# Performance work log

Measured on AMD Instinct MI355X. Metric: run time of the kernel, lower is better.

Reference implementation:

```python
import jax, jax.numpy as jnp
import numpy as np

NEG_SLOPE = 0.2  # PyG GATConv default LeakyReLU slope


def _gat(h, src, dst, num_nodes, W, a_src, a_dst, bias):
    """PyG-style GATConv (concat=True, eval mode, self-loops already in src/dst)."""
    heads, out = a_src.shape
    hp = (h @ W).reshape(num_nodes, heads, out)          # (N, H, F)
    e_s = (hp * a_src).sum(-1)                            # (N, H)
    e_d = (hp * a_dst).sum(-1)                            # (N, H)
    e = jax.nn.leaky_relu(e_s[src] + e_d[dst], NEG_SLOPE)  # (E, H)
    m = jax.ops.segment_max(e, dst, num_segments=num_nodes)
    w = jnp.exp(e - m[dst])
    z = jax.ops.segment_sum(w, dst, num_segments=num_nodes)
    alpha = w / (z[dst] + 1e-16)                          # softmax over in-edges per dst
    agg = jax.ops.segment_sum(hp[src] * alpha[:, :, None], dst, num_segments=num_nodes)
    return agg.reshape(num_nodes, heads * out) + bias


def setup_inputs() -> dict:
    key = jax.random.key(0)
    ks = jax.random.split(key, 20)
    N, T, Fin, H, heads, E = 30000, 4, 256, 64, 4, 240000
    D = H * heads  # 256
    s = 0.05
    p = lambda k, shape: (jax.random.normal(k, shape, jnp.float32) * s)
    return {
        "x": jax.random.normal(ks[0], (N, T, Fin), jnp.float32),
        "edge_index": jax.random.randint(ks[1], (2, E), 0, N, jnp.int32),
        "Wp": p(ks[2], (Fin, H)), "bp": p(ks[3], (H,)),
        "W0": p(ks[4], (H, D)), "a_src0": p(ks[5], (heads, H)), "a_dst0": p(ks[6], (heads, H)), "b0": p(ks[7], (D,)),
        "W1": p(ks[8], (D, D)), "a_src1": p(ks[9], (heads, H)), "a_dst1": p(ks[10], (heads, H)), "b1": p(ks[11], (D,)),
        "Wq": p(ks[12], (D, D)), "bq": p(ks[13], (D,)),
        "Wk": p(ks[14], (D, D)), "bk": p(ks[15], (D,)),
        "Wv": p(ks[16], (D, D)), "bv": p(ks[17], (D,)),
    }


def reference(x, edge_index, Wp, bp, W0, a_src0, a_dst0, b0, W1, a_src1, a_dst1, b1,
              Wq, bq, Wk, bk, Wv, bv):
    N, T, Fin = x.shape
    D = Wq.shape[0]
    loops = jnp.arange(N, dtype=edge_index.dtype)
    src = jnp.concatenate([edge_index[0], loops])  # add self-loops (PyG default)
    dst = jnp.concatenate([edge_index[1], loops])
    xT = jnp.transpose(x, (1, 0, 2))  # (T, N, Fin)

    def step(_, xt):
        h = xt @ Wp + bp
        h = jax.nn.elu(_gat(h, src, dst, N, W0, a_src0, a_dst0, b0))
        h = jax.nn.elu(_gat(h, src, dst, N, W1, a_src1, a_dst1, b1))
        return None, h

    _, embs = jax.lax.scan(step, None, xT)  # (T, N, D)

    # temporal attention
    Q = embs @ Wq + bq
    K = embs @ Wk + bk
    V = embs @ Wv + bv
    Q_time = Q.mean(axis=1)  # (T, D)
    K_time = K.mean(axis=1)  # (T, D)
    scores = (Q_time @ K_time.T) / jnp.sqrt(jnp.asarray(D, jnp.float32))
    attn = jax.nn.softmax(scores, axis=1)            # (T, T)
    Vr = V.reshape(T, -1)                            # (T, N*D)
    attended = attn @ Vr                             # (T, N*D)
    return attended[-1].reshape(N, D)
```

## Files before the change

### kernel.cpp

```cpp
#include <hip/hip_runtime.h>
#include <math.h>

#define NEG_SLOPE 0.2f

typedef __attribute__((ext_vector_type(8))) short short8;
typedef __attribute__((ext_vector_type(4))) float f32x4;

__device__ inline unsigned short f2bf(float f){
  union { float f; unsigned u; } v; v.f = f;
  unsigned r = v.u + 0x7fffu + ((v.u >> 16) & 1u);
  return (unsigned short)(r >> 16);
}
__device__ inline float bf2f(unsigned u){
  union { unsigned u; float f; } v; v.u = u << 16; return v.f;
}

__global__ __launch_bounds__(256) void k_deg_count(const int* __restrict__ dst, int E, int* __restrict__ deg){
  int i = blockIdx.x*256 + threadIdx.x;
  if (i < E) atomicAdd(&deg[dst[i]], 1);
}
__global__ __launch_bounds__(256) void k_scan_blk(const int* __restrict__ deg, int* __restrict__ rowptr,
                                                  int* __restrict__ bsum, int N){
  __shared__ int ws[4];
  int tid = threadIdx.x;
  int i = blockIdx.x*256 + tid;
  int v = (i < N) ? deg[i]+1 : 0;
  int lane = tid & 63, w = tid >> 6;
  int s = v;
  #pragma unroll
  for (int off=1; off<64; off<<=1){
    int u = __shfl_up(s, off);
    if (lane >= off) s += u;
  }
  if (lane == 63) ws[w] = s;
  __syncthreads();
  int woff = 0;
  #pragma unroll
  for (int k=0;k<4;k++) if (k < w) woff += ws[k];
  int incl = s + woff;
  if (i < N) rowptr[i] = incl - v;
  if (tid == 255) bsum[blockIdx.x] = incl;
}
__global__ __launch_bounds__(256) void k_scan_top(int* __restrict__ bsum, int nb, int* __restrict__ rowptrN){
  __shared__ int buf[256];
  int tid = threadIdx.x;
  int v = (tid < nb) ? bsum[tid] : 0;
  buf[tid] = v;
  __syncthreads();
  for (int off=1; off<256; off<<=1){
    int add = (tid >= off) ? buf[tid-off] : 0;
    __syncthreads();
    buf[tid] += add;
    __syncthreads();
  }
  if (tid < nb) bsum[tid] = buf[tid] - v;
  if (tid == 0) rowptrN[0] = buf[255];
}
__global__ __launch_bounds__(256) void k_scan_fix(int* __restrict__ rowptr, const int* __restrict__ bsum,
                                                  int* __restrict__ pos, int* __restrict__ colidx, int N){
  int i = blockIdx.x*256 + threadIdx.x;
  if (i < N){
    int r = rowptr[i] + bsum[blockIdx.x];
    rowptr[i] = r;
    colidx[r] = i;
    pos[i] = r + 1;
  }
}
__global__ __launch_bounds__(256) void k_fill_edges(const int* __restrict__ src, const int* __restrict__ dst,
                                                    int E, int* __restrict__ pos, int* __restrict__ colidx){
  int i = blockIdx.x*256 + threadIdx.x;
  if (i < E){
    int d = dst[i];
    colidx[atomicAdd(&pos[d],1)] = src[i];
  }
}

__global__ __launch_bounds__(256) void k_prep(const float* __restrict__ Wp, const float* __restrict__ W0,
                                              const float* __restrict__ W1, const float* __restrict__ Wv,
                                              const float* __restrict__ as0, const float* __restrict__ ad0,
                                              unsigned short* __restrict__ WpT, unsigned short* __restrict__ W0T4,
                                              unsigned short* __restrict__ W1T, unsigned short* __restrict__ WvT,
                                              float* __restrict__ ahs, float* __restrict__ ahd){
  int idx = blockIdx.x*256 + threadIdx.x;
  if (idx < 16384){
    int k = idx >> 6, p = idx & 63;
    WpT[p*256 + k] = f2bf(Wp[idx]);
  } else if (idx < 32768){
    int i = idx - 16384;
    int h = i >> 12, r = i & 4095, p = r >> 6, k = r & 63;
    W0T4[i] = f2bf(W0[k*256 + h*64 + p]);
  } else if (idx < 98304){
    int i = idx - 32768; int k = i >> 8, p = i & 255;
    W1T[p*256 + k] = f2bf(W1[i]);
  } else if (idx < 163840){
    int i = idx - 98304; int k = i >> 8, p = i & 255;
    WvT[p*256 + k] = f2bf(Wv[i]);
  } else if (idx < 164096){
    int i = idx - 163840;
    int h = i >> 6, d = i & 63;
    float ss = 0.f, sd = 0.f;
    for (int j=0;j<64;j++){
      float w = W0[d*256 + h*64 + j];
      ss += w * as0[h*64 + j];
      sd += w * ad0[h*64 + j];
    }
    ahs[i] = ss; ahd[i] = sd;
  }
}

__global__ __launch_bounds__(256) void k_h0(const float* __restrict__ A,
                                            const unsigned short* __restrict__ Bt,
                                            const float* __restrict__ bias,
                                            unsigned short* __restrict__ C, int M, int Nn){
  int wid = blockIdx.x*4 + (threadIdx.x >> 6);
  int m0 = wid * 64;
  if (m0 >= M) return;
  int lane = threadIdx.x & 63;
  int lr = lane & 15, g = lane >> 4, lk = g*8;
  const float* Arow[4];
  #pragma unroll
  for (int m=0;m<4;m++){
    int row = m0 + m*16 + lr;
    if (row > M-1) row = M-1;
    Arow[m] = A + (size_t)row*256 + lk;
  }
  const unsigned short* Bb = Bt + (size_t)lr*256 + lk;
  f32x4 acc[4][4];
  #pragma unroll
  for (int m=0;m<4;m++)
    #pragma unroll
    for (int n=0;n<4;n++)
      #pragma unroll
      for (int j=0;j<4;j++) acc[m][n][j] = 0.f;

  #pragma unroll 2
  for (int ks=0; ks<8; ks++){
    int k0 = ks*32;
    short8 bfr[4];
    #pragma unroll
    for (int n=0;n<4;n++)
      bfr[n] = *(const short8*)(Bb + (size_t)n*16*256 + k0);
    short8 afr[4];
    #pragma unroll
    for (int m=0;m<4;m++){
      float4 u = *(const float4*)(Arow[m] + k0);
      float4 w = *(const float4*)(Arow[m] + k0 + 4);
      afr[m][0]=(short)f2bf(u.x); afr[m][1]=(short)f2bf(u.y);
      afr[m][2]=(short)f2bf(u.z); afr[m][3]=(short)f2bf(u.w);
      afr[m][4]=(short)f2bf(w.x); afr[m][5]=(short)f2bf(w.y);
      afr[m][6]=(short)f2bf(w.z); afr[m][7]=(short)f2bf(w.w);
    }
    #pragma unroll
    for (int m=0;m<4;m++)
      #pragma unroll
      for (int n=0;n<4;n++)
        acc[m][n] = __builtin_amdgcn_mfma_f32_16x16x32_bf16(afr[m], bfr[n], acc[m][n], 0,0,0);
  }
  #pragma unroll
  for (int n=0;n<4;n++){
    int col = n*16 + lr;
    float bcol = bias[col];
    #pragma unroll
    for (int m=0;m<4;m++){
      #pragma unroll
      for (int j=0;j<4;j++){
        int row = m0 + m*16 + g*4 + j;
        if (row < M){
          int t = row & 3, nn = row >> 2;
          C[(size_t)t*Nn*64 + (size_t)nn*64 + col] = f2bf(acc[m][n][j] + bcol);
        }
      }
    }
  }
}

__global__ __launch_bounds__(256) void k_gat01(const unsigned short* __restrict__ A,
                                               const unsigned short* __restrict__ W0T4,
                                               const float* __restrict__ b0,
                                               const unsigned short* __restrict__ W1T,
                                               unsigned short* __restrict__ hp, int M){
  __shared__ unsigned short H1[64][264];
  __shared__ unsigned short Bls[256][72];
  int tid = threadIdx.x;
  int m0 = blockIdx.x * 64;
  int wave = tid >> 6, lane = tid & 63;
  int lr = lane & 15, g4 = lane >> 4, lk = g4*8;
  int rbase = m0 + wave*16;

  f32x4 acc1[16];
  #pragma unroll
  for (int q=0;q<16;q++)
    #pragma unroll
    for (int j=0;j<4;j++) acc1[q][j] = 0.f;
  int arow = rbase + lr; if (arow > M-1) arow = M-1;
  #pragma unroll
  for (int h=0;h<4;h++){
    short8 afr[2];
    #pragma unroll
    for (int ks=0;ks<2;ks++)
      afr[ks] = *(const short8*)(A + (size_t)arow*256 + h*64 + ks*32 + lk);
    #pragma unroll
    for (int nn=0;nn<4;nn++){
      #pragma unroll
      for (int ks=0;ks<2;ks++){
        short8 bfr = *(const short8*)(W0T4 + ((size_t)h*64 + nn*16 + lr)*64 + ks*32 + lk);
        acc1[h*4+nn] = __builtin_amdgcn_mfma_f32_16x16x32_bf16(afr[ks], bfr, acc1[h*4+nn], 0,0,0);
      }
    }
  }
  #pragma unroll
  for (int q=0;q<16;q++){
    int col = q*16 + lr;
    float bcol = b0[col];
    #pragma unroll
    for (int j=0;j<4;j++){
      float v = acc1[q][j] + bcol;
      v = (v > 0.f) ? v : (__expf(v) - 1.f);
      H1[wave*16 + g4*4 + j][col] = f2bf(v);
    }
  }
  __syncthreads();

  f32x4 acc2[16];
  #pragma unroll
  for (int q=0;q<16;q++)
    #pragma unroll
    for (int j=0;j<4;j++) acc2[q][j] = 0.f;
  for (int k0=0;k0<256;k0+=64){
    #pragma unroll
    for (int it=0; it<8; it++){
      int idx = tid + it*256;
      int p = idx >> 3, ch = (idx & 7)*8;
      *(uint4*)(&Bls[p][ch]) = *(const uint4*)(W1T + (size_t)p*256 + k0 + ch);
    }
    __syncthreads();
    #pragma unroll
    for (int ks=0;ks<2;ks++){
      short8 afr = *(const short8*)(&H1[wave*16 + lr][k0 + ks*32 + lk]);
      #pragma unroll
      for (int q=0;q<16;q++){
        short8 bfr = *(const short8*)(&Bls[q*16 + lr][ks*32 + lk]);
        acc2[q] = __builtin_amdgcn_mfma_f32_16x16x32_bf16(afr, bfr, acc2[q], 0,0,0);
      }
    }
    __syncthreads();
  }
  #pragma unroll
  for (int q=0;q<16;q++){
    int col = q*16 + lr;
    #pragma unroll
    for (int j=0;j<4;j++){
      int row = m0 + wave*16 + g4*4 + j;
      if (row < M)
        hp[(size_t)row*256 + col] = f2bf(acc2[q][j]);
    }
  }
}

__global__ __launch_bounds__(512) void k_gemm_fin(const unsigned short* __restrict__ embs,
                                                  const float* __restrict__ awp,
                                                  const unsigned short* __restrict__ Bt,
                                                  const float* __restrict__ bias,
                                                  float* __restrict__ C, int M){
  constexpr int K = 256, BK = 64, PAD = 8;
  __shared__ unsigned short Als[128][BK+PAD];
  __shared__ unsigned short Bls[256][BK+PAD];
  int tid = threadIdx.x;
  int m0  = blockIdx.x * 128;
  int wave = tid >> 6, lane = tid & 63;
  int wr = wave & 3, wc = wave >> 2;
  int lr = lane & 15, lk = (lane >> 4) * 8;
  float a0=awp[0], a1=awp[1], a2=awp[2], a3=awp[3];
  size_t sl = (size_t)M*256;
  f32x4 acc[2][8];
  #pragma unroll
  for (int m=0;m<2;m++)
    #pragma unroll
    for (int n=0;n<8;n++)
      #pragma unroll
      for (int j=0;j<4;j++) acc[m][n][j] = 0.f;

  for (int k0 = 0; k0 < K; k0 += BK){
    #pragma unroll
    for (int i=0;i<2;i++){
      int idx = tid + i*512;
      int r = idx >> 3, ch = (idx & 7)*8;
      int row = m0 + r;
      uint4 w = make_uint4(0,0,0,0);
      if (row < M){
        size_t o = (size_t)row*256 + k0 + ch;
        uint4 u0 = *(const uint4*)(embs + o);
        uint4 u1 = *(const uint4*)(embs + o + sl);
        uint4 u2 = *(const uint4*)(embs + o + 2*sl);
        uint4 u3 = *(const uint4*)(embs + o + 3*sl);
        const unsigned* p0=&u0.x; const unsigned* p1=&u1.x;
        const unsigned* p2=&u2.x; const unsigned* p3=&u3.x;
        unsigned* pw=&w.x;
        #pragma unroll
        for (int q=0;q<4;q++){
          float lo = a0*bf2f(p0[q]&0xffffu) + a1*bf2f(p1[q]&0xffffu) + a2*bf2f(p2[q]&0xffffu) + a3*bf2f(p3[q]&0xffffu);
          float hi = a0*bf2f(p0[q]>>16)     + a1*bf2f(p1[q]>>16)     + a2*bf2f(p2[q]>>16)     + a3*bf2f(p3[q]>>16);
          pw[q] = (unsigned)f2bf(lo) | ((unsigned)f2bf(hi) << 16);
        }
      }
      *(uint4*)(&Als[r][ch]) = w;
    }
    #pragma unroll
    for (int i=0;i<4;i++){
      int idx = tid + i*512;
      int r = idx >> 3, ch = (idx & 7)*8;
      *(uint4*)(&Bls[r][ch]) = *(const uint4*)(Bt + (size_t)r*K + k0 + ch);
    }
    __syncthreads();
    #pragma unroll
    for (int ks=0; ks<2; ks++){
      short8 afr[2], bfr[8];
      #pragma unroll
      for (int m=0;m<2;m++)
        afr[m] = *(const short8*)(&Als[wr*32 + m*16 + lr][ks*32 + lk]);
      #pragma unroll
      for (int n=0;n<8;n++)
        bfr[n] = *(const short8*)(&Bls[wc*128 + n*16 + lr][ks*32 + lk]);
      #pragma unroll
      for (int m=0;m<2;m++)
        #pragma unroll
        for (int n=0;n<8;n++)
          acc[m][n] = __builtin_amdgcn_mfma_f32_16x16x32_bf16(afr[m], bfr[n], acc[m][n], 0,0,0);
    }
    __syncthreads();
  }
  #pragma unroll
  for (int m=0;m<2;m++){
    #pragma unroll
    for (int n=0;n<8;n++){
      int col = wc*128 + n*16 + lr;
      float bcol = bias[col];
      #pragma unroll
      for (int j=0;j<4;j++){
        int row = m0 + wr*32 + m*16 + (lane>>4)*4 + j;
        if (row < M)
          C[(size_t)row*256 + col] = acc[m][n][j] + bcol;
      }
    }
  }
}

__global__ __launch_bounds__(256) void k_esd0(const unsigned short* __restrict__ h0,
                                              const float* __restrict__ ahs, const float* __restrict__ ahd,
                                              float* __restrict__ e_s, float* __restrict__ e_d, int M){
  int n = blockIdx.x*4 + (threadIdx.x >> 6);
  if (n >= M) return;
  int lane = threadIdx.x & 63;
  int h = lane >> 4, l4 = (lane & 15)*4;
  uint2 v = *(const uint2*)(h0 + (size_t)n*64 + l4);
  float v0 = bf2f(v.x & 0xffffu), v1 = bf2f(v.x >> 16);
  float v2 = bf2f(v.y & 0xffffu), v3 = bf2f(v.y >> 16);
  float4 as = *(const float4*)(ahs + h*64 + l4);
  float4 ad = *(const float4*)(ahd + h*64 + l4);
  float ps = v0*as.x + v1*as.y + v2*as.z + v3*as.w;
  float pd = v0*ad.x + v1*ad.y + v2*ad.z + v3*ad.w;
  #pragma unroll
  for (int off=1; off<16; off<<=1){ ps += __shfl_xor(ps,off); pd += __shfl_xor(pd,off); }
  if ((lane & 15) == 0){
    e_s[n*4+h] = ps; e_d[n*4+h] = pd;
  }
}

__global__ __launch_bounds__(256) void k_agg0(const unsigned short* __restrict__ h0all,
                                              const float* __restrict__ e_s, const float* __restrict__ e_d,
                                              const int* __restrict__ rowptr, const int* __restrict__ colidx,
                                              unsigned short* __restrict__ agg, int N){
  int n = blockIdx.x*4 + (threadIdx.x >> 6);
  if (n >= N) return;
  int t = blockIdx.y;
  int g = t*N + n;
  int lane = threadIdx.x & 63;
  int half = lane >> 5, l = lane & 31;
  int h = l >> 3, di = (l & 7)*8;
  int s0 = rowptr[n], s1 = rowptr[n+1];
  float ed = e_d[(size_t)g*4 + h];
  const unsigned short* h0t = h0all + (size_t)t*N*64;
  const float* est = e_s + (size_t)t*N*4;
  float z = 0.f;
  float a[8] = {0,0,0,0,0,0,0,0};
  int i = s0;
  for (; i+4 <= s1; i += 4){
    int sA = colidx[i + half];
    int sB = colidx[i + 2 + half];
    uint4 vA = *(const uint4*)(h0t + (size_t)sA*64 + di);
    uint4 vB = *(const uint4*)(h0t + (size_t)sB*64 + di);
    float eA = est[sA*4 + h] + ed;
    float eB = est[sB*4 + h] + ed;
    eA = fmaxf(eA, NEG_SLOPE*eA); eB = fmaxf(eB, NEG_SLOPE*eB);
    float wA = __expf(eA), wB = __expf(eB);
    z += wA + wB;
    a[0] += wA*bf2f(vA.x&0xffffu) + wB*bf2f(vB.x&0xffffu);
    a[1] += wA*bf2f(vA.x>>16)     + wB*bf2f(vB.x>>16);
    a[2] += wA*bf2f(vA.y&0xffffu) + wB*bf2f(vB.y&0xffffu);
    a[3] += wA*bf2f(vA.y>>16)     + wB*bf2f(vB.y>>16);
    a[4] += wA*bf2f(vA.z&0xffffu) + wB*bf2f(vB.z&0xffffu);
    a[5] += wA*bf2f(vA.z>>16)     + wB*bf2f(vB.z>>16);
    a[6] += wA*bf2f(vA.w&0xffffu) + wB*bf2f(vB.w&0xffffu);
    a[7] += wA*bf2f(vA.w>>16)     + wB*bf2f(vB.w>>16);
  }
  for (; i+2 <= s1; i += 2){
    int s = colidx[i + half];
    uint4 v = *(const uint4*)(h0t + (size_t)s*64 + di);
    float e = est[s*4 + h] + ed;
    e = fmaxf(e, NEG_SLOPE*e);
    float w = __expf(e);
    z += w;
    a[0] += w*bf2f(v.x&0xffffu); a[1] += w*bf2f(v.x>>16);
    a[2] += w*bf2f(v.y&0xffffu); a[3] += w*bf2f(v.y>>16);
    a[4] += w*bf2f(v.z&0xffffu); a[5] += w*bf2f(v.z>>16);
    a[6] += w*bf2f(v.w&0xffffu); a[7] += w*bf2f(v.w>>16);
  }
  if (i < s1 && half == 0){
    int s = colidx[i];
    uint4 v = *(const uint4*)(h0t + (size_t)s*64 + di);
    float e = est[s*4 + h] + ed;
    e = fmaxf(e, NEG_SLOPE*e);
    float w = __expf(e);
    z += w;
    a[0] += w*bf2f(v.x&0xffffu); a[1] += w*bf2f(v.x>>16);
    a[2] += w*bf2f(v.y&0xffffu); a[3] += w*bf2f(v.y>>16);
    a[4] += w*bf2f(v.z&0xffffu); a[5] += w*bf2f(v.z>>16);
    a[6] += w*bf2f(v.w&0xffffu); a[7] += w*bf2f(v.w>>16);
  }
  z += __shfl_xor(z, 32);
  #pragma unroll
  for (int q=0;q<8;q++) a[q] += __shfl_xor(a[q], 32);
  if (half == 0){
    float inv = 1.f / (z + 1e-16f);
    uint4 r;
    r.x = (unsigned)f2bf(a[0]*inv) | ((unsigned)f2bf(a[1]*inv) << 16);
    r.y = (unsigned)f2bf(a[2]*inv) | ((unsigned)f2bf(a[3]*inv) << 16);
    r.z = (unsigned)f2bf(a[4]*inv) | ((unsigned)f2bf(a[5]*inv) << 16);
    r.w = (unsigned)f2bf(a[6]*inv) | ((unsigned)f2bf(a[7]*inv) << 16);
    *(uint4*)(agg + (size_t)g*256 + l*8) = r;
  }
}

__global__ __launch_bounds__(256) void k_esd(const unsigned short* __restrict__ hp,
                                             const float* __restrict__ a_s, const float* __restrict__ a_d,
                                             float* __restrict__ e_s, float* __restrict__ e_d, int M){
  int n = blockIdx.x*4 + (threadIdx.x >> 6);
  if (n >= M) return;
  int lane = threadIdx.x & 63;
  uint2 v = *(const uint2*)(hp + (size_t)n*256 + lane*4);
  float v0 = bf2f(v.x & 0xffffu), v1 = bf2f(v.x >> 16);
  float v2 = bf2f(v.y & 0xffffu), v3 = bf2f(v.y >> 16);
  float4 as = *(const float4*)(a_s + lane*4);
  float4 ad = *(const float4*)(a_d + lane*4);
  float ps = v0*as.x + v1*as.y + v2*as.z + v3*as.w;
  float pd = v0*ad.x + v1*ad.y + v2*ad.z + v3*ad.w;
  #pragma unroll
  for (int off=1; off<16; off<<=1){ ps += __shfl_xor(ps,off); pd += __shfl_xor(pd,off); }
  if ((lane & 15) == 0){
    int h = lane >> 4;
    e_s[n*4+h] = ps; e_d[n*4+h] = pd;
  }
}

__global__ __launch_bounds__(256) void k_agg(const unsigned short* __restrict__ hpall,
                                             const float* __restrict__ e_s, const float* __restrict__ e_d,
                                             const int* __restrict__ rowptr, const int* __restrict__ colidx,
                                             const float* __restrict__ bias, unsigned short* __restrict__ outb,
                                             int N){
  int n = blockIdx.x*4 + (threadIdx.x >> 6);
  if (n >= N) return;
  int t = blockIdx.y;
  int g = t*N + n;
  int lane = threadIdx.x & 63;
  int half = lane >> 5, l = lane & 31;
  int h = l >> 3, d0 = l*8;
  int s0 = rowptr[n], s1 = rowptr[n+1];
  float ed = e_d[(size_t)g*4 + h];
  const unsigned short* hpt = hpall + (size_t)t*N*256;
  const float* est = e_s + (size_t)t*N*4;
  float z = 0.f;
  float a[8] = {0,0,0,0,0,0,0,0};
  int i = s0;
  for (; i+4 <= s1; i += 4){
    int sA = colidx[i + half];
    int sB = colidx[i + 2 + half];
    uint4 vA = *(const uint4*)(hpt + (size_t)sA*256 + d0);
    uint4 vB = *(const uint4*)(hpt + (size_t)sB*256 + d0);
    float eA = est[sA*4 + h] + ed;
    float eB = est[sB*4 + h] + ed;
    eA = fmaxf(eA, NEG_SLOPE*eA); eB = fmaxf(eB, NEG_SLOPE*eB);
    float wA = __expf(eA), wB = __expf(eB);
    z += wA + wB;
    a[0] += wA*bf2f(vA.x&0xffffu) + wB*bf2f(vB.x&0xffffu);
    a[1] += wA*bf2f(vA.x>>16)     + wB*bf2f(vB.x>>16);
    a[2] += wA*bf2f(vA.y&0xffffu) + wB*bf2f(vB.y&0xffffu);
    a[3] += wA*bf2f(vA.y>>16)     + wB*bf2f(vB.y>>16);
    a[4] += wA*bf2f(vA.z&0xffffu) + wB*bf2f(vB.z&0xffffu);
    a[5] += wA*bf2f(vA.z>>16)     + wB*bf2f(vB.z>>16);
    a[6] += wA*bf2f(vA.w&0xffffu) + wB*bf2f(vB.w&0xffffu);
    a[7] += wA*bf2f(vA.w>>16)     + wB*bf2f(vB.w>>16);
  }
  for (; i+2 <= s1; i += 2){
    int s = colidx[i + half];
    uint4 v = *(const uint4*)(hpt + (size_t)s*256 + d0);
    float e = est[s*4 + h] + ed;
    e = fmaxf(e, NEG_SLOPE*e);
    float w = __expf(e);
    z += w;
    a[0] += w*bf2f(v.x&0xffffu); a[1] += w*bf2f(v.x>>16);
    a[2] += w*bf2f(v.y&0xffffu); a[3] += w*bf2f(v.y>>16);
    a[4] += w*bf2f(v.z&0xffffu); a[5] += w*bf2f(v.z>>16);
    a[6] += w*bf2f(v.w&0xffffu); a[7] += w*bf2f(v.w>>16);
  }
  if (i < s1 && half == 0){
    int s = colidx[i];
    uint4 v = *(const uint4*)(hpt + (size_t)s*256 + d0);
    float e = est[s*4 + h] + ed;
    e = fmaxf(e, NEG_SLOPE*e);
    float w = __expf(e);
    z += w;
    a[0] += w*bf2f(v.x&0xffffu); a[1] += w*bf2f(v.x>>16);
    a[2] += w*bf2f(v.y&0xffffu); a[3] += w*bf2f(v.y>>16);
    a[4] += w*bf2f(v.z&0xffffu); a[5] += w*bf2f(v.z>>16);
    a[6] += w*bf2f(v.w&0xffffu); a[7] += w*bf2f(v.w>>16);
  }
  z += __shfl_xor(z, 32);
  #pragma unroll
  for (int q=0;q<8;q++) a[q] += __shfl_xor(a[q], 32);
  if (half == 0){
    float inv = 1.f / (z + 1e-16f);
    float4 bA = *(const float4*)(bias + d0);
    float4 bB = *(const float4*)(bias + d0 + 4);
    float o[8];
    o[0]=a[0]*inv+bA.x; o[1]=a[1]*inv+bA.y; o[2]=a[2]*inv+bA.z; o[3]=a[3]*inv+bA.w;
    o[4]=a[4]*inv+bB.x; o[5]=a[5]*inv+bB.y; o[6]=a[6]*inv+bB.z; o[7]=a[7]*inv+bB.w;
    #pragma unroll
    for (int q=0;q<8;q++) o[q] = (o[q] > 0.f) ? o[q] : (__expf(o[q]) - 1.f);
    uint4 r;
    r.x = (unsigned)f2bf(o[0]) | ((unsigned)f2bf(o[1]) << 16);
    r.y = (unsigned)f2bf(o[2]) | ((unsigned)f2bf(o[3]) << 16);
    r.z = (unsigned)f2bf(o[4]) | ((unsigned)f2bf(o[5]) << 16);
    r.w = (unsigned)f2bf(o[6]) | ((unsigned)f2bf(o[7]) << 16);
    *(uint4*)(outb + (size_t)g*256 + d0) = r;
  }
}

__global__ __launch_bounds__(256) void k_colsum(const unsigned short* __restrict__ emb, float* __restrict__ sums, int N){
  __shared__ float red[8][256];
  int tid = threadIdx.x;
  int t = blockIdx.x >> 6, chunk = blockIdx.x & 63;
  int rows_per = (N + 63) / 64;
  int r0 = chunk * rows_per;
  int r1 = min(N, r0 + rows_per);
  const unsigned short* base = emb + (size_t)t*N*256;
  int c0 = (tid & 31)*8, rg = tid >> 5;
  float s[8] = {0,0,0,0,0,0,0,0};
  for (int r = r0 + rg; r < r1; r += 8){
    uint4 v = *(const uint4*)(base + (size_t)r*256 + c0);
    s[0] += bf2f(v.x & 0xffffu); s[1] += bf2f(v.x >> 16);
    s[2] += bf2f(v.y & 0xffffu); s[3] += bf2f(v.y >> 16);
    s[4] += bf2f(v.z & 0xffffu); s[5] += bf2f(v.z >> 16);
    s[6] += bf2f(v.w & 0xffffu); s[7] += bf2f(v.w >> 16);
  }
  #pragma unroll
  for (int j=0;j<8;j++) red[rg][c0+j] = s[j];
  __syncthreads();
  float tot = 0.f;
  #pragma unroll
  for (int g=0;g<8;g++) tot += red[g][tid];
  atomicAdd(&sums[t*256 + tid], tot);
}

__global__ __launch_bounds__(256) void k_attn(const float* __restrict__ sum_emb,
                                              const float* __restrict__ Wq, const float* __restrict__ bq,
                                              const float* __restrict__ Wk, const float* __restrict__ bk,
                                              float* __restrict__ aw, int N){
  __shared__ float mean_s[4][256];
  __shared__ float red[256];
  __shared__ float scores_s[4];
  int j = threadIdx.x;
  float invN = 1.0f/(float)N;
  #pragma unroll
  for (int t=0;t<4;t++) mean_s[t][j] = sum_emb[t*256+j]*invN;
  __syncthreads();
  float q3 = bq[j];
  float kt0=bk[j], kt1=bk[j], kt2=bk[j], kt3=bk[j];
  for (int m=0;m<256;m++){
    float wq = Wq[m*256+j];
    float wk = Wk[m*256+j];
    float m0 = mean_s[0][m], m1 = mean_s[1][m], m2 = mean_s[2][m], m3 = mean_s[3][m];
    q3  += m3*wq;
    kt0 += m0*wk; kt1 += m1*wk; kt2 += m2*wk; kt3 += m3*wk;
  }
  float kts0=kt0, kts1=kt1, kts2=kt2, kts3=kt3;
  #pragma unroll
  for (int t=0;t<4;t++){
    float ktv = (t==0)?kts0:((t==1)?kts1:((t==2)?kts2:kts3));
    red[j] = q3*ktv;
    __syncthreads();
    for (int off=128; off>0; off>>=1){
      if (j < off) red[j] += red[j+off];
      __syncthreads();
    }
    if (j==0) scores_s[t] = red[0]*(1.0f/16.0f);
    __syncthreads();
  }
  if (j==0){
    float mx = fmaxf(fmaxf(scores_s[0],scores_s[1]),fmaxf(scores_s[2],scores_s[3]));
    float w0 = __expf(scores_s[0]-mx), w1 = __expf(scores_s[1]-mx),
          w2 = __expf(scores_s[2]-mx), w3 = __expf(scores_s[3]-mx);
    float s = w0+w1+w2+w3;
    aw[0]=w0/s; aw[1]=w1/s; aw[2]=w2/s; aw[3]=w3/s;
  }
}

extern "C" void kernel_launch(void* const* d_in, const int* in_sizes, int n_in,
                              void* d_out, int out_size, void* d_ws, size_t ws_size,
                              hipStream_t stream){
  (void)n_in; (void)out_size; (void)ws_size;
  const float* x   = (const float*)d_in[0];
  const int*   ei  = (const int*)d_in[1];
  const float* Wp  = (const float*)d_in[2];
  const float* bp  = (const float*)d_in[3];
  const float* W0  = (const float*)d_in[4];
  const float* as0 = (const float*)d_in[5];
  const float* ad0 = (const float*)d_in[6];
  const float* b0  = (const float*)d_in[7];
  const float* W1  = (const float*)d_in[8];
  const float* as1 = (const float*)d_in[9];
  const float* ad1 = (const float*)d_in[10];
  const float* b1  = (const float*)d_in[11];
  const float* Wq  = (const float*)d_in[12];
  const float* bq  = (const float*)d_in[13];
  const float* Wk  = (const float*)d_in[14];
  const float* bk  = (const float*)d_in[15];
  const float* Wv  = (const float*)d_in[16];
  const float* bv  = (const float*)d_in[17];
  float* out = (float*)d_out;

  const int T = 4, FIN = 256;
  const int N = in_sizes[0] / (T*FIN);
  const int E = in_sizes[1] / 2;
  const int TN = T*N;
  const int* src = ei;
  const int* dst = ei + E;

  char* ws = (char*)d_ws;
  size_t cur = 0;
  auto alloc = [&](size_t bytes)->void*{
    void* p = ws + cur;
    cur += (bytes + 255) & ~(size_t)255;
    return p;
  };
  unsigned short* h0all = (unsigned short*)alloc((size_t)TN*64*2);
  unsigned short* bufA  = (unsigned short*)alloc((size_t)TN*256*2);
  unsigned short* bufB  = (unsigned short*)alloc((size_t)TN*256*2);
  unsigned short* embs  = (unsigned short*)alloc((size_t)TN*256*2);
  float* e_s    = (float*)alloc((size_t)TN*4*4);
  float* e_d    = (float*)alloc((size_t)TN*4*4);
  float* sume   = (float*)alloc(4*256*4);
  float* aw     = (float*)alloc(256);
  float* ah0s   = (float*)alloc(256*4);
  float* ah0d   = (float*)alloc(256*4);
  int*   rowptr = (int*)alloc((size_t)(N+1)*4);
  int*   deg    = (int*)alloc((size_t)N*4);
  int*   pos    = (int*)alloc((size_t)N*4);
  int*   bsum   = (int*)alloc((size_t)256*4);
  int*   colidx = (int*)alloc((size_t)(E+N)*4);
  unsigned short* WpT  = (unsigned short*)alloc((size_t)64*256*2);
  unsigned short* W0T4 = (unsigned short*)alloc((size_t)4*64*64*2);
  unsigned short* W1T  = (unsigned short*)alloc((size_t)256*256*2);
  unsigned short* WvT  = (unsigned short*)alloc((size_t)256*256*2);

  int nb256 = (N+255)/256;
  int nbE   = (E+255)/256;
  int gmN   = (N+127)/128;
  int gagg  = (TN+3)/4;

  hipMemsetAsync(deg, 0, (size_t)N*4, stream);
  k_deg_count<<<nbE,256,0,stream>>>(dst, E, deg);
  k_scan_blk<<<nb256,256,0,stream>>>(deg, rowptr, bsum, N);
  k_scan_top<<<1,256,0,stream>>>(bsum, nb256, rowptr + N);
  k_scan_fix<<<nb256,256,0,stream>>>(rowptr, bsum, pos, colidx, N);
  k_fill_edges<<<nbE,256,0,stream>>>(src, dst, E, pos, colidx);
  hipMemsetAsync(sume, 0, 4*256*4, stream);

  k_prep<<<641,256,0,stream>>>(Wp, W0, W1, Wv, as0, ad0, WpT, W0T4, W1T, WvT, ah0s, ah0d);

  k_h0<<<(TN/64+3)/4 + 1,256,0,stream>>>(x, WpT, bp, h0all, TN, N);

  k_esd0<<<gagg,256,0,stream>>>(h0all, ah0s, ah0d, e_s, e_d, TN);
  k_agg0<<<dim3((N+3)/4, T),256,0,stream>>>(h0all, e_s, e_d, rowptr, colidx, bufA, N);
  k_gat01<<<(TN+63)/64,256,0,stream>>>(bufA, W0T4, b0, W1T, bufB, TN);
  k_esd<<<gagg,256,0,stream>>>(bufB, as1, ad1, e_s, e_d, TN);
  k_agg<<<dim3((N+3)/4, T),256,0,stream>>>(bufB, e_s, e_d, rowptr, colidx, b1, embs, N);
  k_colsum<<<256,256,0,stream>>>(embs, sume, N);

  k_attn<<<1,256,0,stream>>>(sume, Wq, bq, Wk, bk, aw, N);
  k_gemm_fin<<<gmN,512,0,stream>>>(embs, aw, WvT, bv, out, N);
}
```

Before: 422.1 us.

## Retile fused GAT0/GAT1 kernel into 2x2 wave grid and stream W1 from global

Reorganizes the fused two-GEMM GAT kernel so each wave computes a 32-row by 128-column tile instead of a 16-row by full-width tile. A and B fragments are reused across two row tiles, which halves the B fragment loads per MFMA. The shared-memory staging of W1T and its per-chunk barriers are removed; B fragments are read straight from global/L2. This cuts LDS use and synchronisation, but relies on cache hits for the repeated W1T reads across blocks.

Measured after the change: 438.3 us. +3.8%, slower.

```diff
diff --git a/kernel.cpp b/kernel.cpp
--- a/kernel.cpp
+++ b/kernel.cpp
@@ -180,79 +180,97 @@
                                                const unsigned short* __restrict__ W1T,
                                                unsigned short* __restrict__ hp, int M){
   __shared__ unsigned short H1[64][264];
-  __shared__ unsigned short Bls[256][72];
   int tid = threadIdx.x;
   int m0 = blockIdx.x * 64;
+  if (m0 >= M) return;
   int wave = tid >> 6, lane = tid & 63;
+  int rg = wave & 1;
+  int cg = wave >> 1;
   int lr = lane & 15, g4 = lane >> 4, lk = g4*8;
-  int rbase = m0 + wave*16;
-
-  f32x4 acc1[16];
-  #pragma unroll
-  for (int q=0;q<16;q++)
-    #pragma unroll
-    for (int j=0;j<4;j++) acc1[q][j] = 0.f;
-  int arow = rbase + lr; if (arow > M-1) arow = M-1;
-  #pragma unroll
-  for (int h=0;h<4;h++){
+
+  f32x4 acc[2][8];
+  #pragma unroll
+  for (int r=0;r<2;r++)
+    #pragma unroll
+    for (int c=0;c<8;c++)
+      #pragma unroll
+      for (int j=0;j<4;j++) acc[r][c][j] = 0.f;
+
+  #pragma unroll
+  for (int hh=0; hh<2; hh++){
+    int h = 2*cg + hh;
+    short8 afr[2][2];
+    #pragma unroll
+    for (int rr=0;rr<2;rr++){
+      int row = m0 + rg*32 + rr*16 + lr;
+      if (row > M-1) row = M-1;
+      #pragma unroll
+      for (int ks=0;ks<2;ks++)
+        afr[rr][ks] = *(const short8*)(A + (size_t)row*256 + h*64 + ks*32 + lk);
+    }
+    #pragma unroll
+    for (int qq=0; qq<4; qq++){
+      #pragma unroll
+      for (int ks=0;ks<2;ks++){
+        short8 bfr = *(const short8*)(W0T4 + ((size_t)h*64 + qq*16 + lr)*64 + ks*32 + lk);
+        #pragma unroll
+        for (int rr=0;rr<2;rr++)
+          acc[rr][hh*4+qq] = __builtin_amdgcn_mfma_f32_16x16x32_bf16(afr[rr][ks], bfr, acc[rr][hh*4+qq], 0,0,0);
+      }
+    }
+  }
+  #pragma unroll
+  for (int rr=0;rr<2;rr++){
+    #pragma unroll
+    for (int c=0;c<8;c++){
+      int col = cg*128 + c*16 + lr;
+      float bcol = b0[col];
+      #pragma unroll
+      for (int j=0;j<4;j++){
+        float v = acc[rr][c][j] + bcol;
+        v = (v > 0.f) ? v : (__expf(v) - 1.f);
+        H1[rg*32 + rr*16 + g4*4 + j][col] = f2bf(v);
+      }
+    }
+  }
+  __syncthreads();
+
+  #pragma unroll
+  for (int r=0;r<2;r++)
+    #pragma unroll
+    for (int c=0;c<8;c++)
+      #pragma unroll
+      for (int j=0;j<4;j++) acc[r][c][j] = 0.f;
+
+  const unsigned short* Wb = W1T + (size_t)(cg*128 + lr)*256 + lk;
+  #pragma unroll
+  for (int ks=0; ks<8; ks++){
+    int k0 = ks*32;
     short8 afr[2];
     #pragma unroll
-    for (int ks=0;ks<2;ks++)
-      afr[ks] = *(const short8*)(A + (size_t)arow*256 + h*64 + ks*32 + lk);
-    #pragma unroll
-    for (int nn=0;nn<4;nn++){
-      #pragma unroll
-      for (int ks=0;ks<2;ks++){
-        short8 bfr = *(const short8*)(W0T4 + ((size_t)h*64 + nn*16 + lr)*64 + ks*32 + lk);
-        acc1[h*4+nn] = __builtin_amdgcn_mfma_f32_16x16x32_bf16(afr[ks], bfr, acc1[h*4+nn], 0,0,0);
+    for (int rr=0;rr<2;rr++)
+      afr[rr] = *(const short8*)(&H1[rg*32 + rr*16 + lr][k0 + lk]);
+    short8 bfr[8];
+    #pragma unroll
+    for (int c=0;c<8;c++)
+      bfr[c] = *(const short8*)(Wb + (size_t)c*16*256 + k0);
+    #pragma unroll
+    for (int rr=0;rr<2;rr++)
+      #pragma unroll
+      for (int c=0;c<8;c++)
+        acc[rr][c] = __builtin_amdgcn_mfma_f32_16x16x32_bf16(afr[rr], bfr[c], acc[rr][c], 0,0,0);
+  }
+  #pragma unroll
+  for (int rr=0;rr<2;rr++){
+    #pragma unroll
+    for (int c=0;c<8;c++){
+      int col = cg*128 + c*16 + lr;
+      #pragma unroll
+      for (int j=0;j<4;j++){
+        int row = m0 + rg*32 + rr*16 + g4*4 + j;
+        if (row < M)
+          hp[(size_t)row*256 + col] = f2bf(acc[rr][c][j]);
       }
-    }
-  }
-  #pragma unroll
-  for (int q=0;q<16;q++){
-    int col = q*16 + lr;
-    float bcol = b0[col];
-    #pragma unroll
-    for (int j=0;j<4;j++){
-      float v = acc1[q][j] + bcol;
-      v = (v > 0.f) ? v : (__expf(v) - 1.f);
-      H1[wave*16 + g4*4 + j][col] = f2bf(v);
-    }
-  }
-  __syncthreads();
-
-  f32x4 acc2[16];
-  #pragma unroll
-  for (int q=0;q<16;q++)
-    #pragma unroll
-    for (int j=0;j<4;j++) acc2[q][j] = 0.f;
-  for (int k0=0;k0<256;k0+=64){
-    #pragma unroll
-    for (int it=0; it<8; it++){
-      int idx = tid + it*256;
-      int p = idx >> 3, ch = (idx & 7)*8;
-      *(uint4*)(&Bls[p][ch]) = *(const uint4*)(W1T + (size_t)p*256 + k0 + ch);
-    }
-    __syncthreads();
-    #pragma unroll
-    for (int ks=0;ks<2;ks++){
-      short8 afr = *(const short8*)(&H1[wave*16 + lr][k0 + ks*32 + lk]);
-      #pragma unroll
-      for (int q=0;q<16;q++){
-        short8 bfr = *(const short8*)(&Bls[q*16 + lr][ks*32 + lk]);
-        acc2[q] = __builtin_amdgcn_mfma_f32_16x16x32_bf16(afr, bfr, acc2[q], 0,0,0);
-      }
-    }
-    __syncthreads();
-  }
-  #pragma unroll
-  for (int q=0;q<16;q++){
-    int col = q*16 + lr;
-    #pragma unroll
-    for (int j=0;j<4;j++){
-      int row = m0 + wave*16 + g4*4 + j;
-      if (row < M)
-        hp[(size_t)row*256 + col] = f2bf(acc2[q][j]);
     }
   }
 }
```
